# Kernel optimization log

Measured on AMD Instinct MI355X. Metric: run time of the kernel, lower is better.

Reference implementation:

```python
import jax, jax.numpy as jnp
import numpy as np

N = 50000          # nodes
E = 1600000        # edges (avg degree 32)
DIMS = [128, 128, 128, 64]  # in_features + hidden_dims


def setup_inputs() -> dict:
    key = jax.random.key(0)
    ks = jax.random.split(key, 10)
    x = jax.random.normal(ks[0], (N, DIMS[0]), dtype=jnp.float32)
    edge_index = jax.random.randint(ks[1], (2, E), 0, N, dtype=jnp.int64)
    edge_weight = jax.random.uniform(ks[2], (E,), dtype=jnp.float32)
    params = {}
    for i in range(3):
        fan_in, fan_out = DIMS[i], DIMS[i + 1]
        scale = jnp.sqrt(6.0 / (fan_in + fan_out))  # glorot as in PyG GCNConv lin
        params[f"W{i+1}"] = jax.random.uniform(ks[3 + i], (fan_in, fan_out), jnp.float32, -scale, scale)
        params[f"b{i+1}"] = jnp.zeros((fan_out,), jnp.float32)
    return dict(x=x, edge_index=edge_index, edge_weight=edge_weight, **params)


def gcn_norm(edge_index, edge_weight, n):
    # PyG gcn_norm: add self-loops (weight 1), symmetric deg^-1/2 normalization
    src, dst = edge_index[0], edge_index[1]
    loop = jnp.arange(n, dtype=src.dtype)
    src = jnp.concatenate([src, loop])
    dst = jnp.concatenate([dst, loop])
    ew = jnp.concatenate([edge_weight, jnp.ones((n,), edge_weight.dtype)])
    deg = jax.ops.segment_sum(ew, dst, num_segments=n)  # degree at target
    dinv = jnp.where(deg > 0, jax.lax.rsqrt(jnp.maximum(deg, 1e-30)), 0.0)
    return src, dst, dinv[src] * ew * dinv[dst]


def gcn_conv(x, W, b, src, dst, norm, n):
    h = x @ W                                   # [N, out]
    msg = h[src] * norm[:, None]                # gather + edge scale
    agg = jax.ops.segment_sum(msg, dst, num_segments=n)  # scatter-add to targets
    return agg + b


def reference(x, edge_index, edge_weight, W1, b1, W2, b2, W3, b3):
    n = x.shape[0]
    src, dst, norm = gcn_norm(edge_index, edge_weight, n)
    x = jax.nn.relu(gcn_conv(x, W1, b1, src, dst, norm, n))
    x = jax.nn.relu(gcn_conv(x, W2, b2, src, dst, norm, n))
    return gcn_conv(x, W3, b3, src, dst, norm, n)
```

## Files before the change

### kernel.cpp

```cpp
#include <hip/hip_runtime.h>
#include <hip/hip_bf16.h>
#include <hip/hip_fp16.h>


#define K_IN 128
#define FIX_SCALE 8388608.0f
#define CE 4096

typedef _Float16 f16x8 __attribute__((ext_vector_type(8)));
typedef float f32x4 __attribute__((ext_vector_type(4)));

__global__ __launch_bounds__(1024) void part_count_wt(
    const int* __restrict__ dst, int* __restrict__ counts,
    unsigned short* __restrict__ lrank, int nb, int nblk, int e,
    const float* __restrict__ W1, const float* __restrict__ W2,
    const float* __restrict__ W3, _Float16* __restrict__ Wt1,
    _Float16* __restrict__ Wt2, _Float16* __restrict__ Wt3) {
    int blk = blockIdx.x;
    if (blk >= nblk) {
        int i = (blk - nblk) * 1024 + threadIdx.x;
        if (i < 128 * 128) {
            int k = i >> 7, nn = i & 127;
            Wt1[(size_t)nn * 128 + k] = (_Float16)W1[i];
        } else if (i < 2 * 128 * 128) {
            int j = i - 128 * 128, k = j >> 7, nn = j & 127;
            Wt2[(size_t)nn * 128 + k] = (_Float16)W2[j];
        } else if (i < 2 * 128 * 128 + 64 * 128) {
            int l = i - 2 * 128 * 128, k = l >> 6, nn = l & 63;
            Wt3[(size_t)nn * 128 + k] = (_Float16)W3[l];
        }
        return;
    }
    __shared__ int c[256];
    int t = threadIdx.x;
    for (int i = t; i < nb; i += 1024) c[i] = 0;
    __syncthreads();
    int b0 = blk * CE;
#pragma unroll
    for (int j = 0; j < 4; j++) {
        int i = b0 + j * 1024 + t;
        if (i < e) {
            int b = dst[i] >> 8;
            int r = atomicAdd(&c[b], 1);
            lrank[i] = (unsigned short)r;
        }
    }
    __syncthreads();
    for (int i = t; i < nb; i += 1024) counts[(size_t)i * nblk + blk] = c[i];
}

__global__ __launch_bounds__(256) void reduce_kernel(const int* __restrict__ v,
                                                     int* __restrict__ bs, int m) {
    __shared__ int s[256];
    int t = threadIdx.x, i = blockIdx.x * 256 + t;
    s[t] = (i < m) ? v[i] : 0;
    __syncthreads();
    for (int off = 128; off > 0; off >>= 1) {
        if (t < off) s[t] += s[t + off];
        __syncthreads();
    }
    if (t == 0) bs[blockIdx.x] = s[0];
}

__global__ __launch_bounds__(1024) void scanb1024(const int* __restrict__ bs,
                                                  int* __restrict__ bo, int nbb) {
    __shared__ int s[1024];
    int t = threadIdx.x;
    s[t] = (t < nbb) ? bs[t] : 0;
    __syncthreads();
    for (int off = 1; off < 1024; off <<= 1) {
        int cur = s[t];
        int add = (t >= off) ? s[t - off] : 0;
        __syncthreads();
        s[t] = cur + add;
        __syncthreads();
    }
    if (t < nbb) bo[t] = (t == 0) ? 0 : s[t - 1];
}

__global__ __launch_bounds__(256) void scanw_kernel(const int* __restrict__ v,
                                                    const int* __restrict__ bo,
                                                    int* __restrict__ outp, int m) {
    __shared__ int s[256];
    int t = threadIdx.x, i = blockIdx.x * 256 + t;
    int c = (i < m) ? v[i] : 0;
    s[t] = c;
    __syncthreads();
    for (int off = 1; off < 256; off <<= 1) {
        int cur = s[t];
        int add = (t >= off) ? s[t - off] : 0;
        __syncthreads();
        s[t] = cur + add;
        __syncthreads();
    }
    if (i < m) outp[i] = bo[blockIdx.x] + (s[t] - c);
}

__global__ __launch_bounds__(1024) void part_scatter(const int* __restrict__ src,
                                                     const int* __restrict__ dst,
                                                     const float* __restrict__ ew,
                                                     const int* __restrict__ base,
                                                     const int* __restrict__ counts,
                                                     const unsigned short* __restrict__ lrank,
                                                     int2* __restrict__ arr1,
                                                     int nb, int nblk, int e) {
    __shared__ int hs[256];
    __shared__ int lbase[256];
    __shared__ int gb[256];
    __shared__ unsigned char bb[CE];
    __shared__ int2 buf[CE];
    int t = threadIdx.x, blk = blockIdx.x;

    if (t < 256) hs[t] = (t < nb) ? counts[(size_t)t * nblk + blk] : 0;
    __syncthreads();
    for (int off = 1; off < 256; off <<= 1) {
        int cur = 0, add = 0;
        if (t < 256) { cur = hs[t]; add = (t >= off) ? hs[t - off] : 0; }
        __syncthreads();
        if (t < 256) hs[t] = cur + add;
        __syncthreads();
    }
    if (t < 256) {
        int cnt = (t < nb) ? counts[(size_t)t * nblk + blk] : 0;
        int lb = hs[t] - cnt;
        lbase[t] = lb;
        gb[t] = ((t < nb) ? base[(size_t)t * nblk + blk] : 0) - lb;
    }
    __syncthreads();

    int b0 = blk * CE;
    int nloc = e - b0; if (nloc > CE) nloc = CE;
#pragma unroll
    for (int j = 0; j < 4; j++) {
        int i = b0 + j * 1024 + t;
        if (i < e) {
            int d = dst[i];
            int b = d >> 8;
            int slot = lbase[b] + lrank[i];
            buf[slot] = make_int2((src[i] << 8) | (d & 255), __float_as_int(ew[i]));
            bb[slot] = (unsigned char)b;
        }
    }
    __syncthreads();
#pragma unroll
    for (int j = 0; j < 4; j++) {
        int s = j * 1024 + t;
        if (s < nloc) arr1[gb[bb[s]] + s] = buf[s];
    }
}

#define EPCAP 10240
__global__ __launch_bounds__(1024) void bucket_csr(const int2* __restrict__ arr1,
                                                   const int* __restrict__ base,
                                                   unsigned short* __restrict__ rank2,
                                                   float* __restrict__ dinv,
                                                   int* __restrict__ row_ptr,
                                                   int2* __restrict__ ep,
                                                   int nb, int nblk, int n, int e) {
    __shared__ unsigned long long pk[256];
    __shared__ int nbase[256];
    __shared__ float ldsdinv[256];
    __shared__ int ss[256];
    __shared__ int2 eps[EPCAP];
    int t = threadIdx.x, b = blockIdx.x;
    int beg = base[(size_t)b * nblk];
    int end = (b + 1 < nb) ? base[(size_t)(b + 1) * nblk] : e;
    if (t < 256) pk[t] = 0ULL;
    __syncthreads();
    for (int i = beg + t; i < end; i += 1024) {
        int2 a = arr1[i];
        int ld = a.x & 255;
        float w = __int_as_float(a.y);
        unsigned long long fx = (unsigned long long)(unsigned int)(w * FIX_SCALE + 0.5f);
        unsigned long long old = atomicAdd(&pk[ld], (fx << 32) | 1ULL);
        rank2[i] = (unsigned short)(old & 0xffffffffULL);
    }
    __syncthreads();
    int cnt = (t < 256) ? (int)(pk[t] & 0xffffffffULL) : 0;
    if (t < 256) ss[t] = cnt;
    __syncthreads();
    for (int off = 1; off < 256; off <<= 1) {
        int cur = 0, add = 0;
        if (t < 256) { cur = ss[t]; add = (t >= off) ? ss[t - off] : 0; }
        __syncthreads();
        if (t < 256) ss[t] = cur + add;
        __syncthreads();
    }
    if (t < 256) {
        nbase[t] = ss[t] - cnt;
        int d = b * 256 + t;
        if (d < n) {
            float dv = rsqrtf(1.0f + (float)(unsigned int)(pk[t] >> 32) * (1.0f / FIX_SCALE));
            dinv[d] = dv;
            ldsdinv[t] = dv;
            row_ptr[d] = beg + nbase[t];
        }
    }
    __syncthreads();
    int tot = end - beg;
    if (tot <= EPCAP) {
        for (int i = beg + t; i < end; i += 1024) {
            int2 a = arr1[i];
            int ld = a.x & 255;
            float w = __int_as_float(a.y) * ldsdinv[ld];
            eps[nbase[ld] + rank2[i]] = make_int2(a.x >> 8, __float_as_int(w));
        }
        __syncthreads();
        for (int j = t; j < tot; j += 1024) ep[beg + j] = eps[j];
    } else {
        for (int i = beg + t; i < end; i += 1024) {
            int2 a = arr1[i];
            int ld = a.x & 255;
            int pos = beg + nbase[ld] + rank2[i];
            float w = __int_as_float(a.y) * ldsdinv[ld];
            ep[pos] = make_int2(a.x >> 8, __float_as_int(w));
        }
    }
}

template <int NOUT, bool XF16, bool FUSEVAL>
__global__ __launch_bounds__(256) void mfma_gemm(const void* __restrict__ Xv,
                                                 const _Float16* __restrict__ Wt,
                                                 _Float16* __restrict__ H, int n,
                                                 int gGemm, int vblk,
                                                 int2* __restrict__ ep,
                                                 const float* __restrict__ dinv,
                                                 int* __restrict__ row_ptr, int e) {
    constexpr int CTW = NOUT / 64;
    __shared__ _Float16 Xs[64][136];
    __shared__ _Float16 Ws[NOUT][136];
    int t = threadIdx.x;
    if (FUSEVAL && (int)blockIdx.x >= gGemm) {
        int vb = blockIdx.x - gGemm;
        if (vb == 0 && t == 0) row_ptr[n] = e;
        for (int i = vb * 256 + t; i < e; i += vblk * 256) {
            int2 a = ep[i];
            float w = __int_as_float(a.y) * dinv[a.x];
            ep[i] = make_int2(a.x << 8, __float_as_int(w));
        }
        return;
    }
    int row0 = blockIdx.x * 64;

    for (int i = t * 8; i < NOUT * K_IN; i += 2048) {
        int nn = i >> 7, k = i & 127;
        *(uint4*)&Ws[nn][k] = *(const uint4*)&Wt[i];
    }
    if (XF16) {
        const _Float16* X = (const _Float16*)Xv;
        for (int i = t * 8; i < 64 * K_IN; i += 2048) {
            int r = i >> 7, k = i & 127;
            int row = row0 + r;
            uint4 v = make_uint4(0u, 0u, 0u, 0u);
            if (row < n) v = *(const uint4*)(X + (size_t)row * K_IN + k);
            *(uint4*)&Xs[r][k] = v;
        }
    } else {
        const float* X = (const float*)Xv;
        for (int i = t * 4; i < 64 * K_IN; i += 1024) {
            int r = i >> 7, k = i & 127;
            int row = row0 + r;
            float4 x4 = make_float4(0.f, 0.f, 0.f, 0.f);
            if (row < n) x4 = *(const float4*)(X + (size_t)row * K_IN + k);
            union { _Float16 h[4]; uint2 u; } uu;
            uu.h[0] = (_Float16)x4.x; uu.h[1] = (_Float16)x4.y;
            uu.h[2] = (_Float16)x4.z; uu.h[3] = (_Float16)x4.w;
            *(uint2*)&Xs[r][k] = uu.u;
        }
    }
    __syncthreads();

    int lane = t & 63, w = t >> 6;
    int m = lane & 15, g = lane >> 4;
    f32x4 acc[4][CTW];
#pragma unroll
    for (int mt = 0; mt < 4; mt++)
#pragma unroll
        for (int ct = 0; ct < CTW; ct++) acc[mt][ct] = (f32x4){0.f, 0.f, 0.f, 0.f};

#pragma unroll
    for (int kt = 0; kt < 4; kt++) {
        int kb = kt * 32 + g * 8;
        f16x8 a[4];
#pragma unroll
        for (int mt = 0; mt < 4; mt++) a[mt] = *(const f16x8*)&Xs[mt * 16 + m][kb];
#pragma unroll
        for (int ct = 0; ct < CTW; ct++) {
            int nn = w * (16 * CTW) + ct * 16 + m;
            f16x8 b = *(const f16x8*)&Ws[nn][kb];
#pragma unroll
            for (int mt = 0; mt < 4; mt++)
                acc[mt][ct] = __builtin_amdgcn_mfma_f32_16x16x32_f16(a[mt], b, acc[mt][ct], 0, 0, 0);
        }
    }

#pragma unroll
    for (int mt = 0; mt < 4; mt++) {
#pragma unroll
        for (int r = 0; r < 4; r++) {
            int row = row0 + mt * 16 + g * 4 + r;
            if (row < n) {
#pragma unroll
                for (int ct = 0; ct < CTW; ct++)
                    H[(size_t)row * NOUT + w * (16 * CTW) + ct * 16 + m] =
                        (_Float16)acc[mt][ct][r];
            }
        }
    }
}

template <int F, bool RELU, bool OF16>
__global__ __launch_bounds__(256) void agg_kernel(const __half* __restrict__ H,
                                                  const int* __restrict__ row_ptr,
                                                  const int2* __restrict__ ep,
                                                  const float* __restrict__ dinv,
                                                  const float* __restrict__ bias,
                                                  void* __restrict__ outv, int n) {
    constexpr int UN = 24;
    int wid = threadIdx.x >> 6;
    int lane = threadIdx.x & 63;
    int node = blockIdx.x * 4 + wid;
    if (node >= n) return;

    int start = __builtin_amdgcn_readfirstlane(row_ptr[node]);
    int end   = __builtin_amdgcn_readfirstlane(row_ptr[node + 1]);
    float di = dinv[node];
    float sw = di * di;

    const unsigned lb = (unsigned)lane * (F == 128 ? 4u : 2u);

    float a0, a1;
    if (F == 128) {
        float2 s2 = __half22float2(((const __half2*)(H + (size_t)node * 128))[lane]);
        a0 = s2.x * sw; a1 = s2.y * sw;
    } else {
        a0 = __half2float(H[(size_t)node * 64 + lane]) * sw; a1 = 0.f;
    }

    int len = end - start;
    int nf = len / UN;
    for (int b = 0; b < nf; b++) {
        int p0 = start + b * UN;
        int2 e[UN];
#pragma unroll
        for (int u = 0; u < UN; u++) e[u] = ep[p0 + u];
        __half2 v2[UN];
        __half v1[UN];
#pragma unroll
        for (int u = 0; u < UN; u++) {
            unsigned off = (unsigned)e[u].x;
            if (F == 64) off >>= 1;
            if (F == 128) v2[u] = *(const __half2*)((const char*)H + (off + lb));
            else          v1[u] = *(const __half*)((const char*)H + (off + lb));
        }
#pragma unroll
        for (int u = 0; u < UN; u++) {
            float w = __int_as_float(e[u].y);
            if (F == 128) {
                float2 f = __half22float2(v2[u]);
                a0 += w * f.x; a1 += w * f.y;
            } else {
                a0 += w * __half2float(v1[u]);
            }
        }
    }
    int base = start + nf * UN;
    if (base < end) {
        int2 e[UN];
#pragma unroll
        for (int u = 0; u < UN; u++) {
            int p = base + u;
            int q = (p < end) ? p : end - 1;
            int2 t2 = ep[q];
            if (p >= end) t2.y = 0;
            e[u] = t2;
        }
        __half2 v2[UN];
        __half v1[UN];
#pragma unroll
        for (int u = 0; u < UN; u++) {
            unsigned off = (unsigned)e[u].x;
            if (F == 64) off >>= 1;
            if (F == 128) v2[u] = *(const __half2*)((const char*)H + (off + lb));
            else          v1[u] = *(const __half*)((const char*)H + (off + lb));
        }
#pragma unroll
        for (int u = 0; u < UN; u++) {
            float w = __int_as_float(e[u].y);
            if (F == 128) {
                float2 f = __half22float2(v2[u]);
                a0 += w * f.x; a1 += w * f.y;
            } else {
                a0 += w * __half2float(v1[u]);
            }
        }
    }

    if (F == 128) {
        float o0 = a0 + bias[lane * 2];
        float o1 = a1 + bias[lane * 2 + 1];
        if (RELU) { o0 = fmaxf(o0, 0.f); o1 = fmaxf(o1, 0.f); }
        if (OF16) {
            ((__half2*)outv)[(size_t)node * 64 + lane] = __floats2half2_rn(o0, o1);
        } else {
            *(float2*)((float*)outv + (size_t)node * 128 + lane * 2) = make_float2(o0, o1);
        }
    } else {
        float o = a0 + bias[lane];
        if (RELU) o = fmaxf(o, 0.f);
        if (OF16) ((__half*)outv)[(size_t)node * 64 + lane] = __float2half(o);
        else      ((float*)outv)[(size_t)node * 64 + lane] = o;
    }
}


extern "C" void kernel_launch(void* const* d_in, const int* in_sizes, int n_in,
                              void* d_out, int out_size, void* d_ws, size_t ws_size,
                              hipStream_t stream) {
    const float* x   = (const float*)d_in[0];
    const int*   ei  = (const int*)d_in[1];
    const float* ew  = (const float*)d_in[2];
    const float* W1  = (const float*)d_in[3];
    const float* b1  = (const float*)d_in[4];
    const float* W2  = (const float*)d_in[5];
    const float* b2  = (const float*)d_in[6];
    const float* W3  = (const float*)d_in[7];
    const float* b3  = (const float*)d_in[8];
    float* out = (float*)d_out;

    const int N = in_sizes[0] / K_IN;
    const int E = in_sizes[2];
    const int* src = ei;
    const int* dst = ei + E;

    const int NB   = (N + 255) >> 8;
    const int NBLK = (E + CE - 1) / CE;
    const int M    = NB * NBLK;
    const int NBB  = (M + 255) / 256;
    const int NWT  = (2 * 128 * 128 + 64 * 128 + 1023) / 1024;
    const int VBLK = 1024;

    char* w = (char*)d_ws;
    auto alloc = [&](size_t bytes) {
        void* p = (void*)w;
        w += (bytes + 255) & ~(size_t)255;
        return p;
    };
    int*            counts = (int*)alloc((size_t)M * 4);
    int*            base   = (int*)alloc((size_t)M * 4);
    int*            bsM    = (int*)alloc((size_t)NBB * 4);
    int*            boM    = (int*)alloc((size_t)NBB * 4);
    unsigned short* lrank  = (unsigned short*)alloc((size_t)E * 2);
    int2*           arr1   = (int2*)alloc((size_t)E * 8);
    float*          dinv   = (float*)alloc((size_t)N * 4);
    int*            row_ptr= (int*)alloc((size_t)(N + 1) * 4);
    int2*           ep     = (int2*)alloc((size_t)E * 8);
    _Float16*       Wt1    = (_Float16*)alloc(128 * 128 * 2);
    _Float16*       Wt2    = (_Float16*)alloc(128 * 128 * 2);
    _Float16*       Wt3    = (_Float16*)alloc(64 * 128 * 2);
    _Float16*       bufH   = (_Float16*)alloc((size_t)N * 128 * 2);
    _Float16*       bufX   = (_Float16*)alloc((size_t)N * 128 * 2);

    int gGemm = (N + 63) / 64;
    int gAgg  = (N + 3) / 4;

    part_count_wt<<<NBLK + NWT, 1024, 0, stream>>>(dst, counts, lrank, NB, NBLK, E,
                                                   W1, W2, W3, Wt1, Wt2, Wt3);
    reduce_kernel<<<NBB, 256, 0, stream>>>(counts, bsM, M);
    scanb1024<<<1, 1024, 0, stream>>>(bsM, boM, NBB);
    scanw_kernel<<<NBB, 256, 0, stream>>>(counts, boM, base, M);
    part_scatter<<<NBLK, 1024, 0, stream>>>(src, dst, ew, base, counts, lrank,
                                            arr1, NB, NBLK, E);
    bucket_csr<<<NB, 1024, 0, stream>>>(arr1, base, lrank, dinv, row_ptr, ep,
                                        NB, NBLK, N, E);

    mfma_gemm<128, false, true><<<gGemm + VBLK, 256, 0, stream>>>(
        x, Wt1, bufH, N, gGemm, VBLK, ep, dinv, row_ptr, E);
    agg_kernel<128, true, true><<<gAgg, 256, 0, stream>>>((const __half*)bufH, row_ptr, ep,
                                                          dinv, b1, bufX, N);
    mfma_gemm<128, true, false><<<gGemm, 256, 0, stream>>>(
        bufX, Wt2, bufH, N, gGemm, 0, nullptr, nullptr, nullptr, 0);
    agg_kernel<128, true, true><<<gAgg, 256, 0, stream>>>((const __half*)bufH, row_ptr, ep,
                                                          dinv, b2, bufX, N);
    mfma_gemm<64, true, false><<<gGemm, 256, 0, stream>>>(
        bufX, Wt3, bufH, N, gGemm, 0, nullptr, nullptr, nullptr, 0);
    agg_kernel<64, false, false><<<gAgg, 256, 0, stream>>>((const __half*)bufH, row_ptr, ep,
                                                           dinv, b3, out, N);
}
```

Baseline: 294.0 us.

## Fuse neighbor aggregation with following layer GEMM in one kernel

Adds an agg_gemm kernel that aggregates 64 nodes per block into shared memory (with bias and ReLU), then multiplies by the next layer's weights with MFMA and writes the next H. This removes two launches and the global round trip of the intermediate activation buffer. In exchange, each wave now processes 16 nodes serially, so there is less parallelism to hide gather latency, and shared-memory use per block is higher, which can lower occupancy.

```diff
diff --git a/kernel.cpp b/kernel.cpp
--- a/kernel.cpp
+++ b/kernel.cpp
@@ -309,6 +309,127 @@
     }
 }
 
+template <int NOUT, bool RELU>
+__global__ __launch_bounds__(256) void agg_gemm(const __half* __restrict__ H,
+                                                const int* __restrict__ row_ptr,
+                                                const int2* __restrict__ ep,
+                                                const float* __restrict__ dinv,
+                                                const float* __restrict__ bias,
+                                                const _Float16* __restrict__ Wt,
+                                                _Float16* __restrict__ Hout, int n) {
+    constexpr int CTW = NOUT / 64;
+    constexpr int UN = 24;
+    __shared__ _Float16 Xs[64][136];
+    __shared__ _Float16 Ws[NOUT][136];
+    int t = threadIdx.x;
+    int row0 = blockIdx.x * 64;
+
+    for (int i = t * 8; i < NOUT * K_IN; i += 2048) {
+        int nn = i >> 7, k = i & 127;
+        *(uint4*)&Ws[nn][k] = *(const uint4*)&Wt[i];
+    }
+
+    int wid = t >> 6, lane = t & 63;
+    const unsigned lb = (unsigned)lane * 4u;
+    for (int l = 0; l < 16; l++) {
+        int node = row0 + wid * 16 + l;
+        float o0 = 0.f, o1 = 0.f;
+        if (node < n) {
+            int start = __builtin_amdgcn_readfirstlane(row_ptr[node]);
+            int end   = __builtin_amdgcn_readfirstlane(row_ptr[node + 1]);
+            float di = dinv[node];
+            float sw = di * di;
+            float2 s2 = __half22float2(((const __half2*)(H + (size_t)node * 128))[lane]);
+            float a0 = s2.x * sw, a1 = s2.y * sw;
+
+            int len = end - start;
+            int nf = len / UN;
+            for (int b = 0; b < nf; b++) {
+                int p0 = start + b * UN;
+                int2 e[UN];
+#pragma unroll
+                for (int u = 0; u < UN; u++) e[u] = ep[p0 + u];
+                __half2 v2[UN];
+#pragma unroll
+                for (int u = 0; u < UN; u++)
+                    v2[u] = *(const __half2*)((const char*)H + ((unsigned)e[u].x + lb));
+#pragma unroll
+                for (int u = 0; u < UN; u++) {
+                    float wt = __int_as_float(e[u].y);
+                    float2 f = __half22float2(v2[u]);
+                    a0 += wt * f.x; a1 += wt * f.y;
+                }
+            }
+            int bse = start + nf * UN;
+            if (bse < end) {
+                int2 e[UN];
+#pragma unroll
+                for (int u = 0; u < UN; u++) {
+                    int p = bse + u;
+                    int q = (p < end) ? p : end - 1;
+                    int2 t2 = ep[q];
+                    if (p >= end) t2.y = 0;
+                    e[u] = t2;
+                }
+                __half2 v2[UN];
+#pragma unroll
+                for (int u = 0; u < UN; u++)
+                    v2[u] = *(const __half2*)((const char*)H + ((unsigned)e[u].x + lb));
+#pragma unroll
+                for (int u = 0; u < UN; u++) {
+                    float wt = __int_as_float(e[u].y);
+                    float2 f = __half22float2(v2[u]);
+                    a0 += wt * f.x; a1 += wt * f.y;
+                }
+            }
+            o0 = a0 + bias[lane * 2];
+            o1 = a1 + bias[lane * 2 + 1];
+            if (RELU) { o0 = fmaxf(o0, 0.f); o1 = fmaxf(o1, 0.f); }
+        }
+        union { __half2 h; unsigned u; } r;
+        r.h = __floats2half2_rn(o0, o1);
+        *(unsigned*)&Xs[wid * 16 + l][lane * 2] = r.u;
+    }
+    __syncthreads();
+
+    int m = lane & 15, g = lane >> 4;
+    f32x4 acc[4][CTW];
+#pragma unroll
+    for (int mt = 0; mt < 4; mt++)
+#pragma unroll
+        for (int ct = 0; ct < CTW; ct++) acc[mt][ct] = (f32x4){0.f, 0.f, 0.f, 0.f};
+
+#pragma unroll
+    for (int kt = 0; kt < 4; kt++) {
+        int kb = kt * 32 + g * 8;
+        f16x8 a[4];
+#pragma unroll
+        for (int mt = 0; mt < 4; mt++) a[mt] = *(const f16x8*)&Xs[mt * 16 + m][kb];
+#pragma unroll
+        for (int ct = 0; ct < CTW; ct++) {
+            int nn = wid * (16 * CTW) + ct * 16 + m;
+            f16x8 b = *(const f16x8*)&Ws[nn][kb];
+#pragma unroll
+            for (int mt = 0; mt < 4; mt++)
+                acc[mt][ct] = __builtin_amdgcn_mfma_f32_16x16x32_f16(a[mt], b, acc[mt][ct], 0, 0, 0);
+        }
+    }
+
+#pragma unroll
+    for (int mt = 0; mt < 4; mt++) {
+#pragma unroll
+        for (int r = 0; r < 4; r++) {
+            int row = row0 + mt * 16 + g * 4 + r;
+            if (row < n) {
+#pragma unroll
+                for (int ct = 0; ct < CTW; ct++)
+                    Hout[(size_t)row * NOUT + wid * (16 * CTW) + ct * 16 + m] =
+                        (_Float16)acc[mt][ct][r];
+            }
+        }
+    }
+}
+
 template <int F, bool RELU, bool OF16>
 __global__ __launch_bounds__(256) void agg_kernel(const __half* __restrict__ H,
                                                   const int* __restrict__ row_ptr,
@@ -458,8 +579,8 @@
     _Float16*       Wt1    = (_Float16*)alloc(128 * 128 * 2);
     _Float16*       Wt2    = (_Float16*)alloc(128 * 128 * 2);
     _Float16*       Wt3    = (_Float16*)alloc(64 * 128 * 2);
-    _Float16*       bufH   = (_Float16*)alloc((size_t)N * 128 * 2);
-    _Float16*       bufX   = (_Float16*)alloc((size_t)N * 128 * 2);
+    _Float16*       bufA   = (_Float16*)alloc((size_t)N * 128 * 2);
+    _Float16*       bufB   = (_Float16*)alloc((size_t)N * 128 * 2);
 
     int gGemm = (N + 63) / 64;
     int gAgg  = (N + 3) / 4;
@@ -475,15 +596,11 @@
                                         NB, NBLK, N, E);
 
     mfma_gemm<128, false, true><<<gGemm + VBLK, 256, 0, stream>>>(
-        x, Wt1, bufH, N, gGemm, VBLK, ep, dinv, row_ptr, E);
-    agg_kernel<128, true, true><<<gAgg, 256, 0, stream>>>((const __half*)bufH, row_ptr, ep,
-                                                          dinv, b1, bufX, N);
-    mfma_gemm<128, true, false><<<gGemm, 256, 0, stream>>>(
-        bufX, Wt2, bufH, N, gGemm, 0, nullptr, nullptr, nullptr, 0);
-    agg_kernel<128, true, true><<<gAgg, 256, 0, stream>>>((const __half*)bufH, row_ptr, ep,
-                                                          dinv, b2, bufX, N);
-    mfma_gemm<64, true, false><<<gGemm, 256, 0, stream>>>(
-        bufX, Wt3, bufH, N, gGemm, 0, nullptr, nullptr, nullptr, 0);
-    agg_kernel<64, false, false><<<gAgg, 256, 0, stream>>>((const __half*)bufH, row_ptr, ep,
-                                                           dinv, b3, out, N);
-}
+        x, Wt1, bufA, N, gGemm, VBLK, ep, dinv, row_ptr, E);
+    agg_gemm<128, true><<<gGemm, 256, 0, stream>>>(
+        (const __half*)bufA, row_ptr, ep, dinv, b1, Wt2, bufB, N);
+    agg_gemm<64, true><<<gGemm, 256, 0, stream>>>(
+        (const __half*)bufB, row_ptr, ep, dinv, b2, Wt3, bufA, N);
+    agg_kernel<64, false, false><<<gAgg, 256, 0, stream>>>(
+        (const __half*)bufA, row_ptr, ep, dinv, b3, out, N);
+}
```

Measured after the change: 342.0 us. 1.16x slower.

## Fold edge-weight finalization into first aggregation and widen GEMM tiles to 128 rows

Applied to the files above, without the earlier changes.

The separate pass that multiplied each edge weight by dinv[src] and pre-shifted the source index (previously run as extra blocks of the first GEMM) is removed. The first aggregation kernel now does that computation on the fly and writes the finalized edge records back for the later layers to reuse. The GEMM is also reworked to process 128 rows per block instead of 64, which raises MFMA work per Wt load but doubles LDS and accumulator use and halves the grid size. The first aggregation pays for extra dinv gathers and edge write-back, in exchange for dropping a full read-modify-write pass over the edge array.

```diff
diff --git a/kernel.cpp b/kernel.cpp
--- a/kernel.cpp
+++ b/kernel.cpp
@@ -163,6 +163,7 @@
     __shared__ int ss[256];
     __shared__ int2 eps[EPCAP];
     int t = threadIdx.x, b = blockIdx.x;
+    if (b == 0 && t == 0) row_ptr[n] = e;
     int beg = base[(size_t)b * nblk];
     int end = (b + 1 < nb) ? base[(size_t)(b + 1) * nblk] : e;
     if (t < 256) pk[t] = 0ULL;
@@ -218,29 +219,15 @@
     }
 }
 
-template <int NOUT, bool XF16, bool FUSEVAL>
-__global__ __launch_bounds__(256) void mfma_gemm(const void* __restrict__ Xv,
+template <int NOUT, bool XF16>
+__global__ __launch_bounds__(256) void gemm_wide(const void* __restrict__ Xv,
                                                  const _Float16* __restrict__ Wt,
-                                                 _Float16* __restrict__ H, int n,
-                                                 int gGemm, int vblk,
-                                                 int2* __restrict__ ep,
-                                                 const float* __restrict__ dinv,
-                                                 int* __restrict__ row_ptr, int e) {
+                                                 _Float16* __restrict__ H, int n) {
     constexpr int CTW = NOUT / 64;
-    __shared__ _Float16 Xs[64][136];
+    __shared__ _Float16 Xs[128][136];
     __shared__ _Float16 Ws[NOUT][136];
     int t = threadIdx.x;
-    if (FUSEVAL && (int)blockIdx.x >= gGemm) {
-        int vb = blockIdx.x - gGemm;
-        if (vb == 0 && t == 0) row_ptr[n] = e;
-        for (int i = vb * 256 + t; i < e; i += vblk * 256) {
-            int2 a = ep[i];
-            float w = __int_as_float(a.y) * dinv[a.x];
-            ep[i] = make_int2(a.x << 8, __float_as_int(w));
-        }
-        return;
-    }
-    int row0 = blockIdx.x * 64;
+    int row0 = blockIdx.x * 128;
 
     for (int i = t * 8; i < NOUT * K_IN; i += 2048) {
         int nn = i >> 7, k = i & 127;
@@ -248,7 +235,7 @@
     }
     if (XF16) {
         const _Float16* X = (const _Float16*)Xv;
-        for (int i = t * 8; i < 64 * K_IN; i += 2048) {
+        for (int i = t * 8; i < 128 * K_IN; i += 2048) {
             int r = i >> 7, k = i & 127;
             int row = row0 + r;
             uint4 v = make_uint4(0u, 0u, 0u, 0u);
@@ -257,7 +244,7 @@
         }
     } else {
         const float* X = (const float*)Xv;
-        for (int i = t * 4; i < 64 * K_IN; i += 1024) {
+        for (int i = t * 4; i < 128 * K_IN; i += 1024) {
             int r = i >> 7, k = i & 127;
             int row = row0 + r;
             float4 x4 = make_float4(0.f, 0.f, 0.f, 0.f);
@@ -272,30 +259,30 @@
 
     int lane = t & 63, w = t >> 6;
     int m = lane & 15, g = lane >> 4;
-    f32x4 acc[4][CTW];
-#pragma unroll
-    for (int mt = 0; mt < 4; mt++)
+    f32x4 acc[8][CTW];
+#pragma unroll
+    for (int mt = 0; mt < 8; mt++)
 #pragma unroll
         for (int ct = 0; ct < CTW; ct++) acc[mt][ct] = (f32x4){0.f, 0.f, 0.f, 0.f};
 
 #pragma unroll
     for (int kt = 0; kt < 4; kt++) {
         int kb = kt * 32 + g * 8;
-        f16x8 a[4];
-#pragma unroll
-        for (int mt = 0; mt < 4; mt++) a[mt] = *(const f16x8*)&Xs[mt * 16 + m][kb];
+        f16x8 a[8];
+#pragma unroll
+        for (int mt = 0; mt < 8; mt++) a[mt] = *(const f16x8*)&Xs[mt * 16 + m][kb];
 #pragma unroll
         for (int ct = 0; ct < CTW; ct++) {
             int nn = w * (16 * CTW) + ct * 16 + m;
             f16x8 b = *(const f16x8*)&Ws[nn][kb];
 #pragma unroll
-            for (int mt = 0; mt < 4; mt++)
+            for (int mt = 0; mt < 8; mt++)
                 acc[mt][ct] = __builtin_amdgcn_mfma_f32_16x16x32_f16(a[mt], b, acc[mt][ct], 0, 0, 0);
         }
     }
 
 #pragma unroll
-    for (int mt = 0; mt < 4; mt++) {
+    for (int mt = 0; mt < 8; mt++) {
 #pragma unroll
         for (int r = 0; r < 4; r++) {
             int row = row0 + mt * 16 + g * 4 + r;
@@ -309,10 +296,10 @@
     }
 }
 
-template <int F, bool RELU, bool OF16>
+template <int F, bool RELU, bool OF16, bool VAL>
 __global__ __launch_bounds__(256) void agg_kernel(const __half* __restrict__ H,
                                                   const int* __restrict__ row_ptr,
-                                                  const int2* __restrict__ ep,
+                                                  int2* __restrict__ ep,
                                                   const float* __restrict__ dinv,
                                                   const float* __restrict__ bias,
                                                   void* __restrict__ outv, int n) {
@@ -344,23 +331,46 @@
         int2 e[UN];
 #pragma unroll
         for (int u = 0; u < UN; u++) e[u] = ep[p0 + u];
+        unsigned off[UN];
+        float wf[UN];
+        if (VAL) {
+            float dv[UN];
+#pragma unroll
+            for (int u = 0; u < UN; u++) dv[u] = dinv[e[u].x];
+#pragma unroll
+            for (int u = 0; u < UN; u++) {
+                off[u] = (unsigned)e[u].x << 8;
+                wf[u] = __int_as_float(e[u].y) * dv[u];
+            }
+        } else {
+#pragma unroll
+            for (int u = 0; u < UN; u++) {
+                off[u] = (unsigned)e[u].x;
+                if (F == 64) off[u] >>= 1;
+                wf[u] = __int_as_float(e[u].y);
+            }
+        }
         __half2 v2[UN];
         __half v1[UN];
 #pragma unroll
         for (int u = 0; u < UN; u++) {
-            unsigned off = (unsigned)e[u].x;
-            if (F == 64) off >>= 1;
-            if (F == 128) v2[u] = *(const __half2*)((const char*)H + (off + lb));
-            else          v1[u] = *(const __half*)((const char*)H + (off + lb));
+            if (F == 128) v2[u] = *(const __half2*)((const char*)H + (off[u] + lb));
+            else          v1[u] = *(const __half*)((const char*)H + (off[u] + lb));
+        }
+        if (VAL) {
+            int2 o = make_int2(0, 0);
+#pragma unroll
+            for (int u = 0; u < UN; u++)
+                if (lane == u) o = make_int2((int)off[u], __float_as_int(wf[u]));
+            if (lane < UN) ep[p0 + lane] = o;
         }
 #pragma unroll
         for (int u = 0; u < UN; u++) {
-            float w = __int_as_float(e[u].y);
             if (F == 128) {
                 float2 f = __half22float2(v2[u]);
-                a0 += w * f.x; a1 += w * f.y;
+                a0 += wf[u] * f.x; a1 += wf[u] * f.y;
             } else {
-                a0 += w * __half2float(v1[u]);
+                a0 += wf[u] * __half2float(v1[u]);
             }
         }
     }
@@ -375,23 +385,46 @@
             if (p >= end) t2.y = 0;
             e[u] = t2;
         }
+        unsigned off[UN];
+        float wf[UN];
+        if (VAL) {
+            float dv[UN];
+#pragma unroll
+            for (int u = 0; u < UN; u++) dv[u] = dinv[e[u].x];
+#pragma unroll
+            for (int u = 0; u < UN; u++) {
+                off[u] = (unsigned)e[u].x << 8;
+                wf[u] = __int_as_float(e[u].y) * dv[u];
+            }
+        } else {
+#pragma unroll
+            for (int u = 0; u < UN; u++) {
+                off[u] = (unsigned)e[u].x;
+                if (F == 64) off[u] >>= 1;
+                wf[u] = __int_as_float(e[u].y);
+            }
+        }
         __half2 v2[UN];
         __half v1[UN];
 #pragma unroll
         for (int u = 0; u < UN; u++) {
-            unsigned off = (unsigned)e[u].x;
-            if (F == 64) off >>= 1;
-            if (F == 128) v2[u] = *(const __half2*)((const char*)H + (off + lb));
-            else          v1[u] = *(const __half*)((const char*)H + (off + lb));
+            if (F == 128) v2[u] = *(const __half2*)((const char*)H + (off[u] + lb));
+            else          v1[u] = *(const __half*)((const char*)H + (off[u] + lb));
+        }
+        if (VAL) {
+            int2 o = make_int2(0, 0);
+#pragma unroll
+            for (int u = 0; u < UN; u++)
+                if (lane == u) o = make_int2((int)off[u], __float_as_int(wf[u]));
+            if (lane < UN && base + lane < end) ep[base + lane] = o;
         }
 #pragma unroll
         for (int u = 0; u < UN; u++) {
-            float w = __int_as_float(e[u].y);
             if (F == 128) {
                 float2 f = __half22float2(v2[u]);
-                a0 += w * f.x; a1 += w * f.y;
+                a0 += wf[u] * f.x; a1 += wf[u] * f.y;
             } else {
-                a0 += w * __half2float(v1[u]);
+                a0 += wf[u] * __half2float(v1[u]);
             }
         }
     }
@@ -438,7 +471,6 @@
     const int M    = NB * NBLK;
     const int NBB  = (M + 255) / 256;
     const int NWT  = (2 * 128 * 128 + 64 * 128 + 1023) / 1024;
-    const int VBLK = 1024;
 
     char* w = (char*)d_ws;
     auto alloc = [&](size_t bytes) {
@@ -458,10 +490,10 @@
     _Float16*       Wt1    = (_Float16*)alloc(128 * 128 * 2);
     _Float16*       Wt2    = (_Float16*)alloc(128 * 128 * 2);
     _Float16*       Wt3    = (_Float16*)alloc(64 * 128 * 2);
-    _Float16*       bufH   = (_Float16*)alloc((size_t)N * 128 * 2);
-    _Float16*       bufX   = (_Float16*)alloc((size_t)N * 128 * 2);
-
-    int gGemm = (N + 63) / 64;
+    _Float16*       bufA   = (_Float16*)alloc((size_t)N * 128 * 2);
+    _Float16*       bufB   = (_Float16*)alloc((size_t)N * 128 * 2);
+
+    int gWide = (N + 127) / 128;
     int gAgg  = (N + 3) / 4;
 
     part_count_wt<<<NBLK + NWT, 1024, 0, stream>>>(dst, counts, lrank, NB, NBLK, E,
@@ -474,16 +506,13 @@
     bucket_csr<<<NB, 1024, 0, stream>>>(arr1, base, lrank, dinv, row_ptr, ep,
                                         NB, NBLK, N, E);
 
-    mfma_gemm<128, false, true><<<gGemm + VBLK, 256, 0, stream>>>(
-        x, Wt1, bufH, N, gGemm, VBLK, ep, dinv, row_ptr, E);
-    agg_kernel<128, true, true><<<gAgg, 256, 0, stream>>>((const __half*)bufH, row_ptr, ep,
-                                                          dinv, b1, bufX, N);
-    mfma_gemm<128, true, false><<<gGemm, 256, 0, stream>>>(
-        bufX, Wt2, bufH, N, gGemm, 0, nullptr, nullptr, nullptr, 0);
-    agg_kernel<128, true, true><<<gAgg, 256, 0, stream>>>((const __half*)bufH, row_ptr, ep,
-                                                          dinv, b2, bufX, N);
-    mfma_gemm<64, true, false><<<gGemm, 256, 0, stream>>>(
-        bufX, Wt3, bufH, N, gGemm, 0, nullptr, nullptr, nullptr, 0);
-    agg_kernel<64, false, false><<<gAgg, 256, 0, stream>>>((const __half*)bufH, row_ptr, ep,
-                                                           dinv, b3, out, N);
-}
+    gemm_wide<128, false><<<gWide, 256, 0, stream>>>(x, Wt1, bufA, N);
+    agg_kernel<128, true, true, true><<<gAgg, 256, 0, stream>>>(
+        (const __half*)bufA, row_ptr, ep, dinv, b1, bufB, N);
+    gemm_wide<128, true><<<gWide, 256, 0, stream>>>(bufB, Wt2, bufA, N);
+    agg_kernel<128, true, true, false><<<gAgg, 256, 0, stream>>>(
+        (const __half*)bufA, row_ptr, ep, dinv, b2, bufB, N);
+    gemm_wide<64, true><<<gWide, 256, 0, stream>>>(bufB, Wt3, bufA, N);
+    agg_kernel<64, false, false, false><<<gAgg, 256, 0, stream>>>(
+        (const __half*)bufA, row_ptr, ep, dinv, b3, out, N);
+}
```

Result: slower. 325.4 us (+10.7%).
